# Kernel tuning notes

Measured on AMD Instinct MI355X. Metric: run time of the kernel, lower is better.

Reference implementation:

```python
import jax, jax.numpy as jnp
import numpy as np

Z, H, M, N, Y = 128, 512, 256, 10, 4   # z_size, hidden, mem_vec, mem_size, y_dim
B, T = 2048, 32
SHIFT_IND = np.concatenate([np.roll(np.arange(N), s) for s in (-1, 0, 1)])  # [3*N]


def setup_inputs() -> dict:
    key = jax.random.key(0)
    ks = iter(jax.random.split(key, 48))
    def nrm(shape, s=0.05):
        return jax.random.normal(next(ks), shape, dtype=jnp.float32) * s
    d = {}
    d["z_seq"] = jax.random.normal(next(ks), (B, T, Z), dtype=jnp.float32)
    d["W_ih"] = nrm((4 * H, Z + M)); d["W_hh"] = nrm((4 * H, H))
    d["b_ih"] = jnp.zeros((4 * H,), jnp.float32); d["b_hh"] = jnp.zeros((4 * H,), jnp.float32)
    heads = {"read_key": M, "write_key": M, "erase": M, "add": M, "y": Y,
             "rks": 1, "wks": 1, "rig": 1, "wig": 1, "rsh": 3, "wsh": 3, "rshp": 1, "wshp": 1}
    for nm, o in heads.items():
        d["W_" + nm] = nrm((o, H)); d["b_" + nm] = jnp.zeros((o,), jnp.float32)
    d["memory_init"] = nrm((N, M))
    d["gamma"] = jnp.ones((Z,), jnp.float32)
    d["beta"] = jnp.zeros((Z,), jnp.float32)
    return d


def reference(z_seq, W_ih, W_hh, b_ih, b_hh,
              W_read_key, b_read_key, W_write_key, b_write_key,
              W_erase, b_erase, W_add, b_add, W_y, b_y,
              W_rks, b_rks, W_wks, b_wks, W_rig, b_rig, W_wig, b_wig,
              W_rsh, b_rsh, W_wsh, b_wsh, W_rshp, b_rshp, W_wshp, b_wshp,
              memory_init, gamma, beta):
    Bs, Ts = z_seq.shape[0], z_seq.shape[1]
    eps = 1e-8
    # context norm over the time axis (single task segment), unbiased var as torch
    mu = z_seq.mean(1, keepdims=True)
    sig = jnp.sqrt(z_seq.var(1, ddof=1, keepdims=True) + eps)
    z = (z_seq - mu) / sig * gamma + beta
    z_ext = jnp.concatenate([z, jnp.zeros((Bs, 1, Z), z.dtype)], axis=1)  # t == T step uses zero input
    shift_ind = jnp.asarray(SHIFT_IND)

    def lin(h, W, b):
        return h @ W.T + b

    def cos_sim(key_v, mem):  # key [B,M], mem [B,N,M] -> [B,N]
        dot = jnp.einsum('bm,bnm->bn', key_v, mem)
        kn = jnp.maximum(jnp.linalg.norm(key_v, axis=1, keepdims=True), eps)
        mn = jnp.maximum(jnp.linalg.norm(mem, axis=2), eps)
        return dot / (kn * mn)

    def address(key_v, strength, gate, shift_w, sharpen, w_prev, mem, use_interp):
        # content addressing (exp(s*sim)/sum == softmax), interpolation, circular shift, sharpening
        w = jax.nn.softmax(strength * cos_sim(key_v, mem), axis=1)      # [B,N]
        w = jnp.where(use_interp, gate * w + (1.0 - gate) * w_prev, w)
        w_sh = w[:, shift_ind].reshape(Bs, 3, N)                        # gather per shift
        w = jnp.einsum('bsn,bs->bn', w_sh, shift_w)
        wp = w ** sharpen
        return wp / wp.sum(1, keepdims=True)

    def step(carry, xs):
        h, c, read_vec, mem, w_read, w_write = carry
        z_t, t = xs
        lstm_in = jnp.concatenate([z_t, read_vec], axis=1)              # [B, Z+M]
        gates = lstm_in @ W_ih.T + b_ih + h @ W_hh.T + b_hh
        i, f, g, o = jnp.split(gates, 4, axis=1)
        c = jax.nn.sigmoid(f) * c + jax.nn.sigmoid(i) * jnp.tanh(g)
        h = jax.nn.sigmoid(o) * jnp.tanh(c)
        read_key = jnp.tanh(lin(h, W_read_key, b_read_key))
        write_key = jnp.tanh(lin(h, W_write_key, b_write_key))
        rks = jax.nn.softplus(lin(h, W_rks, b_rks))
        wks = jax.nn.softplus(lin(h, W_wks, b_wks))
        rig = jax.nn.sigmoid(lin(h, W_rig, b_rig))
        wig = jax.nn.sigmoid(lin(h, W_wig, b_wig))
        rsh = jax.nn.softmax(lin(h, W_rsh, b_rsh), axis=1)
        wsh = jax.nn.softmax(lin(h, W_wsh, b_wsh), axis=1)
        rshp = jax.nn.softplus(lin(h, W_rshp, b_rshp)) + 1.0
        wshp = jax.nn.softplus(lin(h, W_wshp, b_wshp)) + 1.0
        erase = jax.nn.sigmoid(lin(h, W_erase, b_erase))
        add = jnp.tanh(lin(h, W_add, b_add))
        y_lin = lin(h, W_y, b_y)
        # read (skipped at t==0; interpolation only for t>1)
        w_read_new = address(read_key, rks, rig, rsh, rshp, w_read, mem, t > 1)
        read_vec = jnp.where(t == 0, jnp.zeros((Bs, M), z_t.dtype),
                             jnp.einsum('bnm,bn->bm', mem, w_read_new))
        w_read = jnp.where(t == 0, w_read, w_read_new)
        # write (every step; interpolation only for t>0)
        w_write = address(write_key, wks, wig, wsh, wshp, w_write, mem, t > 0)
        ww = w_write[:, :, None]
        mem = mem * (1.0 - erase[:, None, :] * ww) + add[:, None, :] * ww
        return (h, c, read_vec, mem, w_read, w_write), y_lin

    carry0 = (jnp.zeros((Bs, H), z.dtype), jnp.zeros((Bs, H), z.dtype),
              jnp.zeros((Bs, M), z.dtype),
              jnp.broadcast_to(memory_init, (Bs, N, M)).astype(z.dtype),
              jnp.zeros((Bs, N), z.dtype), jnp.zeros((Bs, N), z.dtype))
    ts = jnp.arange(Ts + 1)
    _, ys = jax.lax.scan(step, carry0, (jnp.swapaxes(z_ext, 0, 1), ts))
    y_pred_linear = ys[-1]  # output of the final (t == T) step
    return y_pred_linear, jnp.argmax(y_pred_linear, axis=1)
```

## Files before the change

### kernel.cpp

```cpp
#include <hip/hip_runtime.h>
#include <hip/hip_bf16.h>

typedef __attribute__((ext_vector_type(8))) short short8;
typedef __attribute__((ext_vector_type(4))) float f32x4;

#define Bsz   2048
#define Tsz   32
#define Zsz   128
#define Hsz   512
#define Msz   256
#define Nsz   10
#define KDIM  896
#define NGATE 2048
#define NHEAD 1040
#define NHEADP 1152

#define ACT_S ((size_t)Bsz * 768)
#define ZPL_S ((size_t)33 * Bsz * 128)
#define WG_S  ((size_t)NGATE * KDIM)
#define WH_S  ((size_t)NHEADP * Hsz)

__device__ __forceinline__ float sigmoidf_(float x) { return 1.f / (1.f + expf(-x)); }
__device__ __forceinline__ float softplusf_(float x) { return x > 20.f ? x : log1pf(expf(x)); }

__device__ __forceinline__ float wave_sum(float v) {
#pragma unroll
    for (int m = 32; m >= 1; m >>= 1) v += __shfl_xor(v, m, 64);
    return v;
}

__device__ __forceinline__ void split3(float v, __hip_bfloat16& o1, __hip_bfloat16& o2, __hip_bfloat16& o3) {
    o1 = __float2bfloat16(v);
    float r = v - __bfloat162float(o1);
    o2 = __float2bfloat16(r);
    r -= __bfloat162float(o2);
    o3 = __float2bfloat16(r);
}

__device__ __forceinline__ void split3u(float v, unsigned short& a, unsigned short& b, unsigned short& c) {
    __hip_bfloat16 x, y, z;
    split3(v, x, y, z);
    a = *reinterpret_cast<unsigned short*>(&x);
    b = *reinterpret_cast<unsigned short*>(&y);
    c = *reinterpret_cast<unsigned short*>(&z);
}

#define MFMA16(A, B, C) __builtin_amdgcn_mfma_f32_16x16x32_bf16((A), (B), (C), 0, 0, 0)

__device__ __forceinline__ void gload16(const void* g, void* l) {
    __builtin_amdgcn_global_load_lds(
        (const __attribute__((address_space(1))) void*)g,
        (__attribute__((address_space(3))) void*)l, 16, 0, 0);
}


__global__ __launch_bounds__(256) void k_lnorm(
    const float* __restrict__ z_seq, const float* __restrict__ gamma,
    const float* __restrict__ beta, __hip_bfloat16* __restrict__ zb)
{
    int idx = blockIdx.x * 256 + threadIdx.x;
    if (idx >= Bsz * Zsz) return;
    int b = idx >> 7, zi = idx & 127;
    const float* p = z_seq + (size_t)b * Tsz * Zsz + zi;
    float v[32];
    float s = 0.f;
#pragma unroll
    for (int t = 0; t < Tsz; t++) { v[t] = p[t * Zsz]; s += v[t]; }
    float mu = s * (1.f / 32.f);
    float ss = 0.f;
#pragma unroll
    for (int t = 0; t < Tsz; t++) { float d = v[t] - mu; ss += d * d; }
    float rs = rsqrtf(ss * (1.f / 31.f) + 1e-8f);
    float ga = gamma[zi], be = beta[zi];
#pragma unroll
    for (int t = 0; t <= Tsz; t++) {
        float val = (t < Tsz) ? (v[t] - mu) * rs * ga + be : 0.f;
        __hip_bfloat16 a, bq, c;
        split3(val, a, bq, c);
        size_t o = ((size_t)t * Bsz + b) * 128 + zi;
        zb[o] = a; zb[o + ZPL_S] = bq; zb[o + 2 * ZPL_S] = c;
    }
}

__global__ __launch_bounds__(256) void k_prep_wcat(
    const float* __restrict__ W_ih, const float* __restrict__ W_hh,
    const float* __restrict__ b_ih, const float* __restrict__ b_hh,
    __hip_bfloat16* __restrict__ Wt, float* __restrict__ bcat)
{
    int idx = blockIdx.x * 256 + threadIdx.x;
    if (idx >= NGATE * KDIM) return;
    int n = idx / KDIM, k = idx % KDIM;
    int jl = n & 15, g = (n >> 4) & 3, jg = n >> 6;
    int r = g * Hsz + jg * 16 + jl;
    float v = (k < 384) ? W_ih[(size_t)r * 384 + k] : W_hh[(size_t)r * Hsz + (k - 384)];
    __hip_bfloat16 a, b, c;
    split3(v, a, b, c);
    Wt[idx] = a; Wt[idx + WG_S] = b; Wt[idx + 2 * WG_S] = c;
    if (k == 0) bcat[n] = b_ih[r] + b_hh[r];
}

struct HeadP { const float* W[13]; const float* b[13]; };

__global__ __launch_bounds__(256) void k_prep_heads(
    HeadP hp, __hip_bfloat16* __restrict__ Wt, float* __restrict__ bh)
{
    int idx = blockIdx.x * 256 + threadIdx.x;
    if (idx >= NHEADP * Hsz) return;
    int n = idx / Hsz, k = idx % Hsz;
    float v = 0.f;
    if (n < NHEAD) {
        const int offs[14] = {0,256,512,768,1024,1028,1029,1030,1031,1032,1035,1038,1039,1040};
        int h = 0;
        while (n >= offs[h + 1]) h++;
        int local = n - offs[h];
        v = hp.W[h][(size_t)local * Hsz + k];
        if (k == 0) bh[n] = hp.b[h][local];
    } else if (k == 0) bh[n] = 0.f;
    __hip_bfloat16 a, b, c;
    split3(v, a, b, c);
    Wt[idx] = a; Wt[idx + WH_S] = b; Wt[idx + 2 * WH_S] = c;
}

__global__ __launch_bounds__(256) void k_init(
    float* __restrict__ cbuf, float* __restrict__ w_read, float* __restrict__ w_write,
    float* __restrict__ mem, const float* __restrict__ memory_init)
{
    int tid = blockIdx.x * blockDim.x + threadIdx.x;
    int stride = gridDim.x * blockDim.x;
    for (int i = tid; i < Bsz * Hsz; i += stride) cbuf[i] = 0.f;
    for (int i = tid; i < Bsz * Nsz; i += stride) { w_read[i] = 0.f; w_write[i] = 0.f; }
    for (int i = tid; i < Bsz * Nsz * Msz; i += stride) mem[i] = memory_init[i % (Nsz * Msz)];
}


__device__ __forceinline__ void stage_tile(
    uint8_t* smem, int wid, int lane,
    const __hip_bfloat16* aP0, size_t aPlaneStride, int aRowStride, int aColOff, int row0,
    const __hip_bfloat16* bP0, size_t bPlaneStride, int bRowStride, int n00,
    int k0)
{
    const int row4 = lane >> 2;
    const int sch = (lane & 3) ^ (row4 & 3);
    const int koff = sch << 3;
#pragma unroll
    for (int i = 0; i < 9; ++i) {
        int c = wid * 9 + i;
        if (c < 24) {
            int p = c >> 3, rg = c & 7;
            int row = rg * 16 + row4;
            const __hip_bfloat16* g = aP0 + (size_t)p * aPlaneStride +
                (size_t)(row0 + row) * aRowStride + aColOff + k0 + koff;
            gload16(g, smem + p * 8192 + rg * 1024);
        } else {
            int c2 = c - 24;
            int p = c2 >> 2, rg = c2 & 3;
            int row = rg * 16 + row4;
            const __hip_bfloat16* g = bP0 + (size_t)p * bPlaneStride +
                (size_t)(n00 + row) * bRowStride + k0 + koff;
            gload16(g, smem + 24576 + p * 4096 + rg * 1024);
        }
    }
}

template<int NKT>
__global__ __launch_bounds__(256, 2) void k_gates(
    const __hip_bfloat16* __restrict__ zt,
    const __hip_bfloat16* __restrict__ actin,
    const __hip_bfloat16* __restrict__ Wg,
    const float* __restrict__ bcat,
    float* __restrict__ cbuf,
    __hip_bfloat16* __restrict__ actout)
{
    __shared__ __align__(1024) uint8_t smem[36864];
    const int tid = threadIdx.x;
    const int wid = tid >> 6, lane = tid & 63;
    const int fr = lane & 15, kg = lane >> 4;
    const int wr = wid >> 1, wc = wid & 1;
    const int wg = blockIdx.x;
    const int xcd = wg & 7, rr = wg >> 3;
    const int bm = (xcd & 1) * 8 + (rr & 7);
    const int bn = (xcd >> 1) * 8 + (rr >> 3);
    const int row0 = bm * 128, n00 = bn * 64;

    f32x4 acc[4][2];
#pragma unroll
    for (int s = 0; s < 4; ++s)
#pragma unroll
        for (int u = 0; u < 2; ++u) acc[s][u] = f32x4{0.f, 0.f, 0.f, 0.f};

    const int swz = (kg ^ (fr & 3)) << 4;
    constexpr int PA[6] = {0, 0, 1, 0, 1, 2};
    constexpr int PB[6] = {0, 1, 0, 2, 1, 0};

    for (int kt = 0; kt < NKT; ++kt) {
        const int k0 = kt * 32;
        if (k0 < 128)
            stage_tile(smem, wid, lane, zt, ZPL_S, 128, 0, row0, Wg, WG_S, KDIM, n00, k0);
        else
            stage_tile(smem, wid, lane, actin, ACT_S, 768, -128, row0, Wg, WG_S, KDIM, n00, k0);
        __syncthreads();

        short8 af[3][4];
#pragma unroll
        for (int p = 0; p < 3; ++p)
#pragma unroll
            for (int s = 0; s < 4; ++s)
                af[p][s] = *(const short8*)(smem + p * 8192 + (wr * 64 + s * 16 + fr) * 64 + swz);
        short8 bf[3][2];
#pragma unroll
        for (int p = 0; p < 3; ++p)
#pragma unroll
            for (int u = 0; u < 2; ++u)
                bf[p][u] = *(const short8*)(smem + 24576 + p * 4096 + (wc * 32 + u * 16 + fr) * 64 + swz);

#pragma unroll
        for (int pr = 0; pr < 6; ++pr)
#pragma unroll
            for (int s = 0; s < 4; ++s)
#pragma unroll
                for (int u = 0; u < 2; ++u)
                    acc[s][u] = MFMA16(af[PA[pr]][s], bf[PB[pr]][u], acc[s][u]);
        __syncthreads();
    }

    float* G = (float*)smem;
#pragma unroll
    for (int s = 0; s < 4; ++s)
#pragma unroll
        for (int u = 0; u < 2; ++u) {
            int g = wc * 2 + u;
#pragma unroll
            for (int r = 0; r < 4; ++r) {
                int row = wr * 64 + s * 16 + kg * 4 + r;
                G[(g * 128 + row) * 17 + fr] = acc[s][u][r];
            }
        }
    __syncthreads();

#pragma unroll
    for (int i = 0; i < 8; ++i) {
        int p2 = i * 256 + tid;
        int row = p2 >> 4, jl = p2 & 15;
        int m = row0 + row;
        int j = bn * 16 + jl;
        float iv = G[(0 * 128 + row) * 17 + jl] + bcat[n00 +  0 + jl];
        float fv = G[(1 * 128 + row) * 17 + jl] + bcat[n00 + 16 + jl];
        float gv = G[(2 * 128 + row) * 17 + jl] + bcat[n00 + 32 + jl];
        float ov = G[(3 * 128 + row) * 17 + jl] + bcat[n00 + 48 + jl];
        size_t ci = (size_t)m * Hsz + j;
        float co = cbuf[ci];
        float cn = sigmoidf_(fv) * co + sigmoidf_(iv) * tanhf(gv);
        float hn = sigmoidf_(ov) * tanhf(cn);
        cbuf[ci] = cn;
        __hip_bfloat16 h1, h2, h3;
        split3(hn, h1, h2, h3);
        size_t ho = (size_t)m * 768 + 256 + j;
        actout[ho] = h1; actout[ho + ACT_S] = h2; actout[ho + 2 * ACT_S] = h3;
    }
}

__global__ __launch_bounds__(256, 2) void k_heads(
    const __hip_bfloat16* __restrict__ actout,
    const __hip_bfloat16* __restrict__ Wh,
    const float* __restrict__ bh,
    float* __restrict__ headbuf,
    int nOff)
{
    __shared__ __align__(1024) uint8_t smem[36864];
    const int tid = threadIdx.x;
    const int wid = tid >> 6, lane = tid & 63;
    const int fr = lane & 15, kg = lane >> 4;
    const int wr = wid >> 1, wc = wid & 1;
    int bm, bn;
    if (nOff == 0) {
        int lin = blockIdx.y * 16 + blockIdx.x;
        int swz = (lin & 7) * 36 + (lin >> 3);
        bm = swz & 15;
        bn = swz >> 4;
    } else {
        bm = blockIdx.x;
        bn = nOff;
    }
    const int row0 = bm * 128, n00 = bn * 64;

    f32x4 acc[4][2];
#pragma unroll
    for (int s = 0; s < 4; ++s)
#pragma unroll
        for (int u = 0; u < 2; ++u) acc[s][u] = f32x4{0.f, 0.f, 0.f, 0.f};

    const int swzl = (kg ^ (fr & 3)) << 4;
    constexpr int PA[6] = {0, 0, 1, 0, 1, 2};
    constexpr int PB[6] = {0, 1, 0, 2, 1, 0};

    const int NKT = Hsz / 32;
    for (int kt = 0; kt < NKT; ++kt) {
        stage_tile(smem, wid, lane, actout, ACT_S, 768, 256, row0, Wh, WH_S, Hsz, n00, kt * 32);
        __syncthreads();

        short8 af[3][4];
#pragma unroll
        for (int p = 0; p < 3; ++p)
#pragma unroll
            for (int s = 0; s < 4; ++s)
                af[p][s] = *(const short8*)(smem + p * 8192 + (wr * 64 + s * 16 + fr) * 64 + swzl);
        short8 bf[3][2];
#pragma unroll
        for (int p = 0; p < 3; ++p)
#pragma unroll
            for (int u = 0; u < 2; ++u)
                bf[p][u] = *(const short8*)(smem + 24576 + p * 4096 + (wc * 32 + u * 16 + fr) * 64 + swzl);

#pragma unroll
        for (int pr = 0; pr < 6; ++pr)
#pragma unroll
            for (int s = 0; s < 4; ++s)
#pragma unroll
                for (int u = 0; u < 2; ++u)
                    acc[s][u] = MFMA16(af[PA[pr]][s], bf[PB[pr]][u], acc[s][u]);
        __syncthreads();
    }

#pragma unroll
    for (int s = 0; s < 4; ++s)
#pragma unroll
        for (int u = 0; u < 2; ++u) {
            int n = n00 + wc * 32 + u * 16 + fr;
            if (n >= NHEAD) continue;
            float bias = bh[n];
#pragma unroll
            for (int r = 0; r < 4; ++r) {
                int m = row0 + wr * 64 + s * 16 + kg * 4 + r;
                headbuf[(size_t)m * NHEAD + n] = acc[s][u][r] + bias;
            }
        }
}


__device__ inline void compute_address(
    const float dot[10], const float mn[10], float kn, float strength, float gate,
    const float sh[3], float sharp, const float* __restrict__ wprev, bool interp,
    float out[10])
{
    float w[10];
    float mx = -1e30f;
#pragma unroll
    for (int n = 0; n < 10; n++) {
        w[n] = strength * (dot[n] / (kn * mn[n]));
        mx = fmaxf(mx, w[n]);
    }
    float s = 0.f;
#pragma unroll
    for (int n = 0; n < 10; n++) { w[n] = expf(w[n] - mx); s += w[n]; }
    float inv = 1.f / s;
#pragma unroll
    for (int n = 0; n < 10; n++) w[n] *= inv;
    if (interp) {
#pragma unroll
        for (int n = 0; n < 10; n++) w[n] = gate * w[n] + (1.f - gate) * wprev[n];
    }
    float w2[10];
#pragma unroll
    for (int n = 0; n < 10; n++) {
        int np1 = (n + 1) % 10, nm1 = (n + 9) % 10;
        w2[n] = sh[0] * w[np1] + sh[1] * w[n] + sh[2] * w[nm1];
    }
    float ssum = 0.f;
#pragma unroll
    for (int n = 0; n < 10; n++) { w2[n] = powf(w2[n], sharp); ssum += w2[n]; }
    float rinv = 1.f / ssum;
#pragma unroll
    for (int n = 0; n < 10; n++) out[n] = w2[n] * rinv;
}

__global__ __launch_bounds__(64) void k_addr3(
    const float* __restrict__ headbuf,
    float* __restrict__ mem,
    float* __restrict__ w_read, float* __restrict__ w_write,
    __hip_bfloat16* __restrict__ actout,
    int t)
{
    const int b = blockIdx.x;
    const int lane = threadIdx.x;
    const float eps = 1e-8f;
    const float* hb = headbuf + (size_t)b * NHEAD;
    float* memb = mem + (size_t)b * Nsz * Msz;

    float4 rk = *reinterpret_cast<const float4*>(hb + lane * 4);
    float4 wk = *reinterpret_cast<const float4*>(hb + 256 + lane * 4);
    float4 er = *reinterpret_cast<const float4*>(hb + 512 + lane * 4);
    float4 ad = *reinterpret_cast<const float4*>(hb + 768 + lane * 4);
    float4 mreg[10];
#pragma unroll
    for (int n = 0; n < 10; n++)
        mreg[n] = *reinterpret_cast<const float4*>(memb + n * Msz + lane * 4);

    rk.x = tanhf(rk.x); rk.y = tanhf(rk.y); rk.z = tanhf(rk.z); rk.w = tanhf(rk.w);
    wk.x = tanhf(wk.x); wk.y = tanhf(wk.y); wk.z = tanhf(wk.z); wk.w = tanhf(wk.w);
    er.x = sigmoidf_(er.x); er.y = sigmoidf_(er.y); er.z = sigmoidf_(er.z); er.w = sigmoidf_(er.w);
    ad.x = tanhf(ad.x); ad.y = tanhf(ad.y); ad.z = tanhf(ad.z); ad.w = tanhf(ad.w);

    float knr = fmaxf(sqrtf(wave_sum(rk.x*rk.x + rk.y*rk.y + rk.z*rk.z + rk.w*rk.w)), eps);
    float knw = fmaxf(sqrtf(wave_sum(wk.x*wk.x + wk.y*wk.y + wk.z*wk.z + wk.w*wk.w)), eps);

    float dotr[10], dotw[10], mn[10];
#pragma unroll
    for (int n = 0; n < 10; n++) {
        float4 m4 = mreg[n];
        dotr[n] = wave_sum(rk.x*m4.x + rk.y*m4.y + rk.z*m4.z + rk.w*m4.w);
        dotw[n] = wave_sum(wk.x*m4.x + wk.y*m4.y + wk.z*m4.z + wk.w*m4.w);
        mn[n]   = fmaxf(sqrtf(wave_sum(m4.x*m4.x + m4.y*m4.y + m4.z*m4.z + m4.w*m4.w)), eps);
    }

    float rks = softplusf_(hb[1028]);
    float wks = softplusf_(hb[1029]);
    float rig = sigmoidf_(hb[1030]);
    float wig = sigmoidf_(hb[1031]);
    float rsh[3], wsh[3];
    {
        float a0 = hb[1032], a1 = hb[1033], a2 = hb[1034];
        float mx = fmaxf(a0, fmaxf(a1, a2));
        float e0 = expf(a0 - mx), e1 = expf(a1 - mx), e2 = expf(a2 - mx);
        float inv = 1.f / (e0 + e1 + e2);
        rsh[0] = e0 * inv; rsh[1] = e1 * inv; rsh[2] = e2 * inv;
        a0 = hb[1035]; a1 = hb[1036]; a2 = hb[1037];
        mx = fmaxf(a0, fmaxf(a1, a2));
        e0 = expf(a0 - mx); e1 = expf(a1 - mx); e2 = expf(a2 - mx);
        inv = 1.f / (e0 + e1 + e2);
        wsh[0] = e0 * inv; wsh[1] = e1 * inv; wsh[2] = e2 * inv;
    }
    float rshp = softplusf_(hb[1038]) + 1.f;
    float wshp = softplusf_(hb[1039]) + 1.f;

    float wfr[10], wfw[10];
    compute_address(dotr, mn, knr, rks, rig, rsh, rshp, w_read + (size_t)b * Nsz, t > 1, wfr);
    compute_address(dotw, mn, knw, wks, wig, wsh, wshp, w_write + (size_t)b * Nsz, t > 0, wfw);

    {
        float4 rv = {0.f, 0.f, 0.f, 0.f};
#pragma unroll
        for (int n = 0; n < 10; n++) {
            float wn = wfr[n];
            rv.x += mreg[n].x * wn; rv.y += mreg[n].y * wn;
            rv.z += mreg[n].z * wn; rv.w += mreg[n].w * wn;
        }
        if (t == 0) rv = float4{0.f, 0.f, 0.f, 0.f};
        ushort4 u1, u2, u3;
        split3u(rv.x, u1.x, u2.x, u3.x);
        split3u(rv.y, u1.y, u2.y, u3.y);
        split3u(rv.z, u1.z, u2.z, u3.z);
        split3u(rv.w, u1.w, u2.w, u3.w);
        size_t o = (size_t)b * 768 + lane * 4;
        *reinterpret_cast<ushort4*>(actout + o)             = u1;
        *reinterpret_cast<ushort4*>(actout + o + ACT_S)     = u2;
        *reinterpret_cast<ushort4*>(actout + o + 2 * ACT_S) = u3;
    }
    if (lane < 10) {
        if (t != 0) w_read[(size_t)b * Nsz + lane] = wfr[lane];
        w_write[(size_t)b * Nsz + lane] = wfw[lane];
    }
#pragma unroll
    for (int n = 0; n < 10; n++) {
        float wwn = wfw[n];
        float4 m4 = mreg[n];
        float4 o4;
        o4.x = m4.x * (1.f - er.x * wwn) + ad.x * wwn;
        o4.y = m4.y * (1.f - er.y * wwn) + ad.y * wwn;
        o4.z = m4.z * (1.f - er.z * wwn) + ad.z * wwn;
        o4.w = m4.w * (1.f - er.w * wwn) + ad.w * wwn;
        *reinterpret_cast<float4*>(memb + n * Msz + lane * 4) = o4;
    }
}

__global__ __launch_bounds__(64) void k_out(
    const float* __restrict__ headbuf, float* __restrict__ d_out)
{
    int b = blockIdx.x * 64 + threadIdx.x;
    if (b >= Bsz) return;
    float4 y = *reinterpret_cast<const float4*>(headbuf + (size_t)b * NHEAD + 1024);
    d_out[(size_t)b * 4 + 0] = y.x;
    d_out[(size_t)b * 4 + 1] = y.y;
    d_out[(size_t)b * 4 + 2] = y.z;
    d_out[(size_t)b * 4 + 3] = y.w;
    int idx = 0; float best = y.x;
    if (y.y > best) { best = y.y; idx = 1; }
    if (y.z > best) { best = y.z; idx = 2; }
    if (y.w > best) { best = y.w; idx = 3; }
    d_out[Bsz * 4 + b] = (float)idx;
}


extern "C" void kernel_launch(void* const* d_in, const int* in_sizes, int n_in,
                              void* d_out, int out_size, void* d_ws, size_t ws_size,
                              hipStream_t stream) {
    const float* z_seq = (const float*)d_in[0];
    const float* W_ih  = (const float*)d_in[1];
    const float* W_hh  = (const float*)d_in[2];
    const float* b_ih  = (const float*)d_in[3];
    const float* b_hh  = (const float*)d_in[4];
    const float* memory_init = (const float*)d_in[31];
    const float* gamma = (const float*)d_in[32];
    const float* beta  = (const float*)d_in[33];

    HeadP hp;
    for (int i = 0; i < 13; i++) {
        hp.W[i] = (const float*)d_in[5 + 2 * i];
        hp.b[i] = (const float*)d_in[6 + 2 * i];
    }

    char* ws = (char*)d_ws;
    size_t off = 0;
    auto alloc = [&](size_t bytes) -> void* {
        off = (off + 255) & ~(size_t)255;
        void* p = ws + off;
        off += bytes;
        return p;
    };
    __hip_bfloat16* zbuf  = (__hip_bfloat16*)alloc(3 * ZPL_S * 2);
    __hip_bfloat16* act   = (__hip_bfloat16*)alloc(2 * 3 * ACT_S * 2);
    float* cbuf    = (float*)alloc((size_t)Bsz * Hsz * 4);
    float* mem     = (float*)alloc((size_t)Bsz * Nsz * Msz * 4);
    float* w_read  = (float*)alloc((size_t)Bsz * Nsz * 4);
    float* w_write = (float*)alloc((size_t)Bsz * Nsz * 4);
    float* headbuf = (float*)alloc((size_t)Bsz * NHEAD * 4);
    __hip_bfloat16* Wg = (__hip_bfloat16*)alloc(3 * WG_S * 2);
    float* bcat    = (float*)alloc((size_t)NGATE * 4);
    __hip_bfloat16* Wh = (__hip_bfloat16*)alloc(3 * WH_S * 2);
    float* bhead   = (float*)alloc((size_t)NHEADP * 4);

    k_prep_wcat<<<(NGATE * KDIM + 255) / 256, 256, 0, stream>>>(W_ih, W_hh, b_ih, b_hh, Wg, bcat);
    k_prep_heads<<<(NHEADP * Hsz + 255) / 256, 256, 0, stream>>>(hp, Wh, bhead);
    k_lnorm<<<(Bsz * Zsz + 255) / 256, 256, 0, stream>>>(z_seq, gamma, beta, zbuf);
    k_init<<<2048, 256, 0, stream>>>(cbuf, w_read, w_write, mem, memory_init);

    float* out_f = (float*)d_out;
    for (int t = 0; t < Tsz; t++) {
        const __hip_bfloat16* ain = act + (size_t)(t & 1) * 3 * ACT_S;
        __hip_bfloat16*       aout = act + (size_t)((t + 1) & 1) * 3 * ACT_S;
        if (t == 0)
            k_gates<4><<<512, 256, 0, stream>>>(
                zbuf, ain, Wg, bcat, cbuf, aout);
        else
            k_gates<28><<<512, 256, 0, stream>>>(
                zbuf + (size_t)t * Bsz * 128, ain, Wg, bcat, cbuf, aout);
        k_heads<<<dim3(16, 18), 256, 0, stream>>>(aout, Wh, bhead, headbuf, 0);
        k_addr3<<<Bsz, 64, 0, stream>>>(headbuf, mem, w_read, w_write, aout, t);
    }
    {
        const int t = Tsz;
        const __hip_bfloat16* ain = act + (size_t)(t & 1) * 3 * ACT_S;
        __hip_bfloat16*       aout = act + (size_t)((t + 1) & 1) * 3 * ACT_S;
        k_gates<28><<<512, 256, 0, stream>>>(
            zbuf + (size_t)t * Bsz * 128, ain, Wg, bcat, cbuf, aout);
        k_heads<<<dim3(16, 1), 256, 0, stream>>>(aout, Wh, bhead, headbuf, 16);
        k_out<<<Bsz / 64, 64, 0, stream>>>(headbuf, out_f);
    }
}
```

Baseline: 3.458 ms.

## Double GEMM K-tile to 64 with wider XOR swizzle and trim heads grid

```diff
diff --git a/kernel.cpp b/kernel.cpp
--- a/kernel.cpp
+++ b/kernel.cpp
@@ -133,31 +133,30 @@
 }
 
 
-__device__ __forceinline__ void stage_tile(
+__device__ __forceinline__ void stage_tile64(
     uint8_t* smem, int wid, int lane,
     const __hip_bfloat16* aP0, size_t aPlaneStride, int aRowStride, int aColOff, int row0,
     const __hip_bfloat16* bP0, size_t bPlaneStride, int bRowStride, int n00,
     int k0)
 {
-    const int row4 = lane >> 2;
-    const int sch = (lane & 3) ^ (row4 & 3);
-    const int koff = sch << 3;
-#pragma unroll
-    for (int i = 0; i < 9; ++i) {
-        int c = wid * 9 + i;
-        if (c < 24) {
-            int p = c >> 3, rg = c & 7;
-            int row = rg * 16 + row4;
+    const int rloc = lane >> 3;
+    const int koff = ((lane & 7) ^ (rloc & 7)) << 3;
+#pragma unroll
+    for (int i = 0; i < 18; ++i) {
+        int c = wid * 18 + i;
+        if (c < 48) {
+            int p = c >> 4, rg = c & 15;
+            int row = rg * 8 + rloc;
             const __hip_bfloat16* g = aP0 + (size_t)p * aPlaneStride +
                 (size_t)(row0 + row) * aRowStride + aColOff + k0 + koff;
-            gload16(g, smem + p * 8192 + rg * 1024);
+            gload16(g, smem + p * 16384 + rg * 1024);
         } else {
-            int c2 = c - 24;
-            int p = c2 >> 2, rg = c2 & 3;
-            int row = rg * 16 + row4;
+            int c2 = c - 48;
+            int p = c2 >> 3, rg = c2 & 7;
+            int row = rg * 8 + rloc;
             const __hip_bfloat16* g = bP0 + (size_t)p * bPlaneStride +
                 (size_t)(n00 + row) * bRowStride + k0 + koff;
-            gload16(g, smem + 24576 + p * 4096 + rg * 1024);
+            gload16(g, smem + 49152 + p * 8192 + rg * 1024);
         }
     }
 }
@@ -171,7 +170,7 @@
     float* __restrict__ cbuf,
     __hip_bfloat16* __restrict__ actout)
 {
-    __shared__ __align__(1024) uint8_t smem[36864];
+    __shared__ __align__(1024) uint8_t smem[73728];
     const int tid = threadIdx.x;
     const int wid = tid >> 6, lane = tid & 63;
     const int fr = lane & 15, kg = lane >> 4;
@@ -188,38 +187,42 @@
 #pragma unroll
         for (int u = 0; u < 2; ++u) acc[s][u] = f32x4{0.f, 0.f, 0.f, 0.f};
 
-    const int swz = (kg ^ (fr & 3)) << 4;
+    const int frs = fr & 7;
     constexpr int PA[6] = {0, 0, 1, 0, 1, 2};
     constexpr int PB[6] = {0, 1, 0, 2, 1, 0};
 
     for (int kt = 0; kt < NKT; ++kt) {
-        const int k0 = kt * 32;
+        const int k0 = kt * 64;
         if (k0 < 128)
-            stage_tile(smem, wid, lane, zt, ZPL_S, 128, 0, row0, Wg, WG_S, KDIM, n00, k0);
+            stage_tile64(smem, wid, lane, zt, ZPL_S, 128, 0, row0, Wg, WG_S, KDIM, n00, k0);
         else
-            stage_tile(smem, wid, lane, actin, ACT_S, 768, -128, row0, Wg, WG_S, KDIM, n00, k0);
+            stage_tile64(smem, wid, lane, actin, ACT_S, 768, -128, row0, Wg, WG_S, KDIM, n00, k0);
         __syncthreads();
 
-        short8 af[3][4];
-#pragma unroll
-        for (int p = 0; p < 3; ++p)
-#pragma unroll
-            for (int s = 0; s < 4; ++s)
-                af[p][s] = *(const short8*)(smem + p * 8192 + (wr * 64 + s * 16 + fr) * 64 + swz);
-        short8 bf[3][2];
-#pragma unroll
-        for (int p = 0; p < 3; ++p)
-#pragma unroll
-            for (int u = 0; u < 2; ++u)
-                bf[p][u] = *(const short8*)(smem + 24576 + p * 4096 + (wc * 32 + u * 16 + fr) * 64 + swz);
-
-#pragma unroll
-        for (int pr = 0; pr < 6; ++pr)
-#pragma unroll
-            for (int s = 0; s < 4; ++s)
+#pragma unroll
+        for (int h = 0; h < 2; ++h) {
+            const int cofs = (((h << 2) + kg) ^ frs) << 4;
+            short8 af[3][4];
+#pragma unroll
+            for (int p = 0; p < 3; ++p)
+#pragma unroll
+                for (int s = 0; s < 4; ++s)
+                    af[p][s] = *(const short8*)(smem + p * 16384 + (wr * 64 + s * 16 + fr) * 128 + cofs);
+            short8 bf[3][2];
+#pragma unroll
+            for (int p = 0; p < 3; ++p)
 #pragma unroll
                 for (int u = 0; u < 2; ++u)
-                    acc[s][u] = MFMA16(af[PA[pr]][s], bf[PB[pr]][u], acc[s][u]);
+                    bf[p][u] = *(const short8*)(smem + 49152 + p * 8192 + (wc * 32 + u * 16 + fr) * 128 + cofs);
+
+#pragma unroll
+            for (int pr = 0; pr < 6; ++pr)
+#pragma unroll
+                for (int s = 0; s < 4; ++s)
+#pragma unroll
+                    for (int u = 0; u < 2; ++u)
+                        acc[s][u] = MFMA16(af[PA[pr]][s], bf[PB[pr]][u], acc[s][u]);
+        }
         __syncthreads();
     }
 
@@ -266,7 +269,7 @@
     float* __restrict__ headbuf,
     int nOff)
 {
-    __shared__ __align__(1024) uint8_t smem[36864];
+    __shared__ __align__(1024) uint8_t smem[73728];
     const int tid = threadIdx.x;
     const int wid = tid >> 6, lane = tid & 63;
     const int fr = lane & 15, kg = lane >> 4;
@@ -274,7 +277,7 @@
     int bm, bn;
     if (nOff == 0) {
         int lin = blockIdx.y * 16 + blockIdx.x;
-        int swz = (lin & 7) * 36 + (lin >> 3);
+        int swz = (lin & 7) * 34 + (lin >> 3);
         bm = swz & 15;
         bn = swz >> 4;
     } else {
@@ -289,35 +292,39 @@
 #pragma unroll
         for (int u = 0; u < 2; ++u) acc[s][u] = f32x4{0.f, 0.f, 0.f, 0.f};
 
-    const int swzl = (kg ^ (fr & 3)) << 4;
+    const int frs = fr & 7;
     constexpr int PA[6] = {0, 0, 1, 0, 1, 2};
     constexpr int PB[6] = {0, 1, 0, 2, 1, 0};
 
-    const int NKT = Hsz / 32;
+    const int NKT = Hsz / 64;
     for (int kt = 0; kt < NKT; ++kt) {
-        stage_tile(smem, wid, lane, actout, ACT_S, 768, 256, row0, Wh, WH_S, Hsz, n00, kt * 32);
+        stage_tile64(smem, wid, lane, actout, ACT_S, 768, 256, row0, Wh, WH_S, Hsz, n00, kt * 64);
         __syncthreads();
 
-        short8 af[3][4];
-#pragma unroll
-        for (int p = 0; p < 3; ++p)
-#pragma unroll
-            for (int s = 0; s < 4; ++s)
-                af[p][s] = *(const short8*)(smem + p * 8192 + (wr * 64 + s * 16 + fr) * 64 + swzl);
-        short8 bf[3][2];
-#pragma unroll
-        for (int p = 0; p < 3; ++p)
-#pragma unroll
-            for (int u = 0; u < 2; ++u)
-                bf[p][u] = *(const short8*)(smem + 24576 + p * 4096 + (wc * 32 + u * 16 + fr) * 64 + swzl);
-
-#pragma unroll
-        for (int pr = 0; pr < 6; ++pr)
-#pragma unroll
-            for (int s = 0; s < 4; ++s)
+#pragma unroll
+        for (int h = 0; h < 2; ++h) {
+            const int cofs = (((h << 2) + kg) ^ frs) << 4;
+            short8 af[3][4];
+#pragma unroll
+            for (int p = 0; p < 3; ++p)
+#pragma unroll
+                for (int s = 0; s < 4; ++s)
+                    af[p][s] = *(const short8*)(smem + p * 16384 + (wr * 64 + s * 16 + fr) * 128 + cofs);
+            short8 bf[3][2];
+#pragma unroll
+            for (int p = 0; p < 3; ++p)
 #pragma unroll
                 for (int u = 0; u < 2; ++u)
-                    acc[s][u] = MFMA16(af[PA[pr]][s], bf[PB[pr]][u], acc[s][u]);
+                    bf[p][u] = *(const short8*)(smem + 49152 + p * 8192 + (wc * 32 + u * 16 + fr) * 128 + cofs);
+
+#pragma unroll
+            for (int pr = 0; pr < 6; ++pr)
+#pragma unroll
+                for (int s = 0; s < 4; ++s)
+#pragma unroll
+                    for (int u = 0; u < 2; ++u)
+                        acc[s][u] = MFMA16(af[PA[pr]][s], bf[PB[pr]][u], acc[s][u]);
+        }
         __syncthreads();
     }
 
@@ -538,19 +545,19 @@
         const __hip_bfloat16* ain = act + (size_t)(t & 1) * 3 * ACT_S;
         __hip_bfloat16*       aout = act + (size_t)((t + 1) & 1) * 3 * ACT_S;
         if (t == 0)
-            k_gates<4><<<512, 256, 0, stream>>>(
+            k_gates<2><<<512, 256, 0, stream>>>(
                 zbuf, ain, Wg, bcat, cbuf, aout);
         else
-            k_gates<28><<<512, 256, 0, stream>>>(
+            k_gates<14><<<512, 256, 0, stream>>>(
                 zbuf + (size_t)t * Bsz * 128, ain, Wg, bcat, cbuf, aout);
-        k_heads<<<dim3(16, 18), 256, 0, stream>>>(aout, Wh, bhead, headbuf, 0);
+        k_heads<<<dim3(16, 17), 256, 0, stream>>>(aout, Wh, bhead, headbuf, 0);
         k_addr3<<<Bsz, 64, 0, stream>>>(headbuf, mem, w_read, w_write, aout, t);
     }
     {
         const int t = Tsz;
         const __hip_bfloat16* ain = act + (size_t)(t & 1) * 3 * ACT_S;
         __hip_bfloat16*       aout = act + (size_t)((t + 1) & 1) * 3 * ACT_S;
-        k_gates<28><<<512, 256, 0, stream>>>(
+        k_gates<14><<<512, 256, 0, stream>>>(
             zbuf + (size_t)t * Bsz * 128, ain, Wg, bcat, cbuf, aout);
         k_heads<<<dim3(16, 1), 256, 0, stream>>>(aout, Wh, bhead, headbuf, 16);
         k_out<<<Bsz / 64, 64, 0, stream>>>(headbuf, out_f);
```

Measured after the change: 3.771 ms. +9.1%, slower.
